# Optimization experiments

Measured on AMD Instinct MI355X. Metric: run time of the kernel, lower is better.

Reference implementation:

```python
import jax, jax.numpy as jnp
import numpy as np

NUM_BANDS = 31
POOL_SIZES = (4, 8, 16)
GN_GROUPS = 32
GN_EPS = 1e-5


def _interp_matrix(out_size, in_size):
    # PyTorch bilinear, align_corners=False, as a sparse-ish [out, in] matrix
    i = np.arange(out_size)
    src = (i + 0.5) * (in_size / out_size) - 0.5
    src = np.clip(src, 0.0, in_size - 1)
    lo = np.floor(src).astype(np.int64)
    hi = np.minimum(lo + 1, in_size - 1)
    w = src - lo
    M = np.zeros((out_size, in_size), dtype=np.float32)
    np.add.at(M, (i, lo), 1.0 - w)
    np.add.at(M, (i, hi), w)
    return jnp.asarray(M)


def _scale_branch(x, s, conv_w, spectral_w):
    # x: [B, C, H, W]; adaptive avg pool to (s, s) == uniform pooling (H, W % s == 0)
    B, C, H, W = x.shape
    xp = x.reshape(B, C, s, H // s, s, W // s).mean(axis=(3, 5))  # [B, C, s, s]
    qkv = jnp.einsum('bchw,oc->bohw', xp, conv_w)  # 1x1 conv, no bias
    rd = conv_w.shape[0] // 3
    q, k, v = qkv[:, :rd], qkv[:, rd:2 * rd], qkv[:, 2 * rd:]
    g = rd // NUM_BANDS  # bands_per_group
    S = s * s
    q = q.reshape(B, g, NUM_BANDS, S).transpose(0, 3, 1, 2)  # [B, S, g, n]
    k = k.reshape(B, g, NUM_BANDS, S).transpose(0, 3, 2, 1)  # [B, S, n, g]
    v = v.reshape(B, g, NUM_BANDS, S).transpose(0, 3, 1, 2)  # [B, S, g, n]
    scale = g ** (-0.5)
    attn = jnp.einsum('bsgn,nm,bsmh->bsgh', q, spectral_w, k) * scale  # [B, S, g, g]
    attn = jax.nn.softmax(attn, axis=-1)
    out = jnp.einsum('bsgh,bshn->bsgn', attn, v)  # [B, S, g, n]
    out = out.transpose(0, 2, 3, 1).reshape(B, rd, s, s)
    Mh = _interp_matrix(H, s)
    Mw = _interp_matrix(W, s)
    return jnp.einsum('bcij,hi,wj->bchw', out, Mh, Mw)  # bilinear upsample to [B, rd, H, W]


def _group_norm(x, weight, bias):
    B, C, H, W = x.shape
    xg = x.reshape(B, GN_GROUPS, C // GN_GROUPS, H, W)
    mean = xg.mean(axis=(2, 3, 4), keepdims=True)
    var = ((xg - mean) ** 2).mean(axis=(2, 3, 4), keepdims=True)
    xn = ((xg - mean) * jax.lax.rsqrt(var + GN_EPS)).reshape(B, C, H, W)
    return xn * weight[None, :, None, None] + bias[None, :, None, None]


def setup_inputs() -> dict:
    key = jax.random.key(0)
    ks = jax.random.split(key, 12)
    B, C, H, W = 4, 256, 256, 256
    rd = 93  # reduced_dim for dim=256, reduction=4, num_bands=31
    x = jax.random.normal(ks[0], (B, C, H, W), dtype=jnp.float32)
    conv_ws = [jax.random.normal(ks[1 + i], (3 * rd, C), dtype=jnp.float32) * (C ** -0.5) for i in range(3)]
    sws = [jnp.eye(NUM_BANDS, dtype=jnp.float32) * 0.1
           + 0.01 * jax.random.normal(ks[4 + i], (NUM_BANDS, NUM_BANDS), dtype=jnp.float32) for i in range(3)]
    fusion_w = jax.random.normal(ks[7], (C, 3 * rd), dtype=jnp.float32) * ((3 * rd) ** -0.5)
    fusion_b = jax.random.normal(ks[8], (C,), dtype=jnp.float32) * 0.01
    gn_w = jnp.ones((C,), dtype=jnp.float32) + 0.01 * jax.random.normal(ks[9], (C,), dtype=jnp.float32)
    gn_b = 0.01 * jax.random.normal(ks[10], (C,), dtype=jnp.float32)
    return {'x': x, 'conv_w0': conv_ws[0], 'conv_w1': conv_ws[1], 'conv_w2': conv_ws[2],
            'sw0': sws[0], 'sw1': sws[1], 'sw2': sws[2],
            'fusion_w': fusion_w, 'fusion_b': fusion_b, 'gn_w': gn_w, 'gn_b': gn_b}


def reference(x, conv_w0, conv_w1, conv_w2, sw0, sw1, sw2, fusion_w, fusion_b, gn_w, gn_b):
    conv_ws = (conv_w0, conv_w1, conv_w2)
    sws = (sw0, sw1, sw2)
    scale_outputs = [_scale_branch(x, s, cw, sw) for s, cw, sw in zip(POOL_SIZES, conv_ws, sws)]
    fused = jnp.concatenate(scale_outputs, axis=1)  # [B, 3*rd, H, W]
    out = jnp.einsum('bchw,oc->bohw', fused, fusion_w) + fusion_b[None, :, None, None]
    return _group_norm(out + x, gn_w, gn_b)
```

## Files before the change

### kernel.cpp

```cpp
#include <hip/hip_runtime.h>
#include <hip/hip_bf16.h>
#include <math.h>

#define B 4
#define C 256
#define H 256
#define Wd 256

__global__ __launch_bounds__(256) void xreadproj_kernel(
    const float* __restrict__ x,
    float* __restrict__ pool16, float* __restrict__ xp16o,
    float* __restrict__ xp8o, float* __restrict__ xp4o,
    float* __restrict__ sx) {

    __shared__ float P0[16][72];
    __shared__ float SS16[16][68];
    __shared__ float SS8[16][72];
    __shared__ float SS4[16][80];
    __shared__ float Rs[16 * 29];
    __shared__ float rs[4][2];

    int bc = blockIdx.x;
    int t = threadIdx.x;
    int wg = t >> 6, l = t & 63;

    const float4* xp = (const float4*)(x + (size_t)bc * (H * Wd));

    for (int e = t; e < 576; e += 256) {
        int r = e / 36, g = e - r * 36;
        if (g < 8)       P0[r][64 + g] = 0.f;
        else if (g < 10) SS16[r][g - 8] = 0.f;
        else if (g < 12) SS16[r][56 + g] = 0.f;
        else if (g < 16) SS8[r][g - 12] = 0.f;
        else if (g < 20) SS8[r][52 + g] = 0.f;
        else if (g < 28) SS4[r][g - 20] = 0.f;
        else             SS4[r][44 + g] = 0.f;
    }

    float a16, b16, a8, b8, a4, b4;
    {
        float w0 = 4.f * (float)l + 0.5f;
        float s16v = w0 * 0.0625f - 0.5f;
        if (l <= 1 || l >= 62) { a16 = 0.f; b16 = 0.f; }
        else { a16 = s16v - floorf(s16v); b16 = 0.0625f; }
        float s8v = w0 * 0.03125f - 0.5f;
        if (l <= 3 || l >= 60) { a8 = 0.f; b8 = 0.f; }
        else { a8 = s8v - floorf(s8v); b8 = 0.03125f; }
        float s4v = w0 * 0.015625f - 0.5f;
        if (l <= 7 || l >= 56) { a4 = 0.f; b4 = 0.f; }
        else { a4 = s4v - floorf(s4v); b4 = 0.015625f; }
    }

    const int i16 = t >> 4, j16 = t & 15;
    const int i8 = t >> 3, j8 = t & 7;
    const int i4 = (t - 64) >> 2, j4 = (t - 64) & 3;

    float accA = 0.f;
    float accB = 0.f;
    float sx1 = 0.f, sx2 = 0.f;

    float4 v[4], vn[4];
#pragma unroll
    for (int it = 0; it < 4; ++it)
        v[it] = xp[(wg * 4 + it) * 64 + l];

#pragma unroll 1
    for (int k = 0; k < 16; ++k) {
        if (k > 0) {
            int kk = k - 1;
            if (kk >= i16 - 1 && kk <= i16 + 1) {
#pragma unroll
                for (int rl = 0; rl < 16; ++rl) {
                    float src = ((float)(kk * 16 + rl) + 0.5f) * 0.0625f - 0.5f;
                    src = fminf(fmaxf(src, 0.f), 15.f);
                    int lo = (int)src; float fr = src - (float)lo;
                    float w = (i16 == lo) ? (1.f - fr) : ((i16 == lo + 1) ? fr : 0.f);
                    accA += w * Rs[rl * 29 + j16];
                }
            }
            if (t < 64) {
                if (kk >= 2 * i8 - 1 && kk <= 2 * i8 + 2) {
#pragma unroll
                    for (int rl = 0; rl < 16; ++rl) {
                        float src = ((float)(kk * 16 + rl) + 0.5f) * 0.03125f - 0.5f;
                        src = fminf(fmaxf(src, 0.f), 7.f);
                        int lo = (int)src; float fr = src - (float)lo;
                        float w = (i8 == lo) ? (1.f - fr) : ((i8 == lo + 1) ? fr : 0.f);
                        accB += w * Rs[rl * 29 + 16 + j8];
                    }
                }
            } else if (t < 80) {
                if (kk >= 4 * i4 - 2 && kk <= 4 * i4 + 5) {
#pragma unroll
                    for (int rl = 0; rl < 16; ++rl) {
                        float src = ((float)(kk * 16 + rl) + 0.5f) * 0.015625f - 0.5f;
                        src = fminf(fmaxf(src, 0.f), 3.f);
                        int lo = (int)src; float fr = src - (float)lo;
                        float w = (i4 == lo) ? (1.f - fr) : ((i4 == lo + 1) ? fr : 0.f);
                        accB += w * Rs[rl * 29 + 24 + j4];
                    }
                }
            }
        }

#pragma unroll
        for (int it = 0; it < 4; ++it) {
            int r = wg * 4 + it;
            float4 vv = v[it];
            float p0 = (vv.x + vv.y) + (vv.z + vv.w);
            float pw = fmaf(3.f, vv.w, fmaf(2.f, vv.z, vv.y));
            sx1 += p0;
            sx2 += vv.x * vv.x + vv.y * vv.y + vv.z * vv.z + vv.w * vv.w;
            P0[r][l]       = p0;
            SS16[r][2 + l] = fmaf(b16, pw, a16 * p0);
            SS8[r][4 + l]  = fmaf(b8,  pw, a8  * p0);
            SS4[r][8 + l]  = fmaf(b4,  pw, a4  * p0);
        }

        if (k < 15) {
#pragma unroll
            for (int it = 0; it < 4; ++it)
                vn[it] = xp[((k + 1) * 16 + wg * 4 + it) * 64 + l];
        }
        __syncthreads();

        for (int tk = t; tk < 464; tk += 256) {
            if (tk < 256) {
                int r = tk >> 4, j = tk & 15;
                float sum = 0.f;
#pragma unroll
                for (int q = 0; q < 4; ++q)
                    sum += P0[r][4 * j + 2 + q] - SS16[r][4 * j + 4 + q];
#pragma unroll
                for (int q = 0; q < 4; ++q) sum += SS16[r][4 * j + q];
                if (j == 0) sum += (P0[r][0] - SS16[r][2]) + (P0[r][1] - SS16[r][3]);
                Rs[r * 29 + j] = sum;
            } else if (tk < 384) {
                int q2 = tk - 256; int r = q2 >> 3, j = q2 & 7;
                float sum = 0.f;
#pragma unroll
                for (int q = 0; q < 8; ++q)
                    sum += P0[r][8 * j + 4 + q] - SS8[r][8 * j + 8 + q];
#pragma unroll
                for (int q = 0; q < 8; ++q) sum += SS8[r][8 * j + q];
                if (j == 0) {
#pragma unroll
                    for (int q = 0; q < 4; ++q) sum += P0[r][q] - SS8[r][4 + q];
                }
                Rs[r * 29 + 16 + j] = sum;
            } else if (tk < 448) {
                int q2 = tk - 384; int r = q2 >> 2, j = q2 & 3;
                float sum = 0.f;
#pragma unroll
                for (int q = 0; q < 16; ++q)
                    sum += P0[r][16 * j + 8 + q] - SS4[r][16 * j + 16 + q];
#pragma unroll
                for (int q = 0; q < 16; ++q) sum += SS4[r][16 * j + q];
                if (j == 0) {
#pragma unroll
                    for (int q = 0; q < 8; ++q) sum += P0[r][q] - SS4[r][8 + q];
                }
                Rs[r * 29 + 24 + j] = sum;
            } else {
                int j = tk - 448;
                float sum = 0.f;
#pragma unroll
                for (int r2 = 0; r2 < 16; ++r2) {
#pragma unroll
                    for (int q = 0; q < 4; ++q) sum += P0[r2][4 * j + q];
                }
                pool16[(size_t)bc * 256 + k * 16 + j] = sum * (1.f / 256.f);
            }
        }
        __syncthreads();
#pragma unroll
        for (int it = 0; it < 4; ++it) v[it] = vn[it];
    }

    {
        int kk = 15;
        if (kk >= i16 - 1 && kk <= i16 + 1) {
#pragma unroll
            for (int rl = 0; rl < 16; ++rl) {
                float src = ((float)(kk * 16 + rl) + 0.5f) * 0.0625f - 0.5f;
                src = fminf(fmaxf(src, 0.f), 15.f);
                int lo = (int)src; float fr = src - (float)lo;
                float w = (i16 == lo) ? (1.f - fr) : ((i16 == lo + 1) ? fr : 0.f);
                accA += w * Rs[rl * 29 + j16];
            }
        }
        if (t < 64) {
            if (kk >= 2 * i8 - 1 && kk <= 2 * i8 + 2) {
#pragma unroll
                for (int rl = 0; rl < 16; ++rl) {
                    float src = ((float)(kk * 16 + rl) + 0.5f) * 0.03125f - 0.5f;
                    src = fminf(fmaxf(src, 0.f), 7.f);
                    int lo = (int)src; float fr = src - (float)lo;
                    float w = (i8 == lo) ? (1.f - fr) : ((i8 == lo + 1) ? fr : 0.f);
                    accB += w * Rs[rl * 29 + 16 + j8];
                }
            }
        } else if (t < 80) {
            if (kk >= 4 * i4 - 2 && kk <= 4 * i4 + 5) {
#pragma unroll
                for (int rl = 0; rl < 16; ++rl) {
                    float src = ((float)(kk * 16 + rl) + 0.5f) * 0.015625f - 0.5f;
                    src = fminf(fmaxf(src, 0.f), 3.f);
                    int lo = (int)src; float fr = src - (float)lo;
                    float w = (i4 == lo) ? (1.f - fr) : ((i4 == lo + 1) ? fr : 0.f);
                    accB += w * Rs[rl * 29 + 24 + j4];
                }
            }
        }
    }

    xp16o[(size_t)bc * 256 + t] = accA;
    if (t < 64) xp8o[(size_t)bc * 64 + t] = accB;
    else if (t < 80) xp4o[(size_t)bc * 16 + (t - 64)] = accB;

#pragma unroll
    for (int off = 1; off < 64; off <<= 1) {
        sx1 += __shfl_xor(sx1, off);
        sx2 += __shfl_xor(sx2, off);
    }
    if (l == 0) { rs[wg][0] = sx1; rs[wg][1] = sx2; }
    __syncthreads();
    if (t == 0) {
        sx[bc * 2]     = rs[0][0] + rs[1][0] + rs[2][0] + rs[3][0];
        sx[bc * 2 + 1] = rs[0][1] + rs[1][1] + rs[2][1] + rs[3][1];
    }
}

__global__ __launch_bounds__(256) void site_kernel(
    const float* __restrict__ pool16,
    const float* __restrict__ cw0, const float* __restrict__ cw1,
    const float* __restrict__ cw2,
    const float* __restrict__ sw0, const float* __restrict__ sw1,
    const float* __restrict__ sw2,
    const float* __restrict__ fusion_w,
    float* __restrict__ y4, float* __restrict__ y8, float* __restrict__ y16) {

    __shared__ float P[256];
    __shared__ float Wm[961];
    __shared__ float QKV[279];
    __shared__ float QW[93];
    __shared__ float A[9];
    __shared__ float OUTV[93];

    int t = threadIdx.x;
    int blk = blockIdx.x;
    int b = blk / 336;
    int r = blk % 336;

    int s, site, foff;
    const float* cw; const float* sw; float* yout;
    if (r < 256)      { s = 16; site = r;       cw = cw2; sw = sw2; foff = 186; yout = y16; }
    else if (r < 320) { s = 8;  site = r - 256; cw = cw1; sw = sw1; foff = 93;  yout = y8;  }
    else              { s = 4;  site = r - 320; cw = cw0; sw = sw0; foff = 0;   yout = y4;  }
    int i = site / s, j = site % s;

    for (int idx = t; idx < 961; idx += 256) Wm[idx] = sw[idx];

    {
        int f = 16 / s;
        float acc = 0.f;
        int base = (b * 256 + t) * 256;
        for (int ii = 0; ii < f; ++ii)
            for (int jj = 0; jj < f; ++jj)
                acc += pool16[base + (i * f + ii) * 16 + (j * f + jj)];
        P[t] = acc / (float)(f * f);
    }
    __syncthreads();

    for (int o = t; o < 279; o += 256) {
        const float4* wrow = (const float4*)(cw + o * 256);
        float acc = 0.f;
#pragma unroll 8
        for (int c4 = 0; c4 < 64; ++c4) {
            float4 wv = wrow[c4];
            acc += wv.x * P[c4 * 4] + wv.y * P[c4 * 4 + 1] +
                   wv.z * P[c4 * 4 + 2] + wv.w * P[c4 * 4 + 3];
        }
        QKV[o] = acc;
    }
    __syncthreads();

    if (t < 93) {
        int g = t / 31, m = t % 31;
        float acc = 0.f;
        for (int n = 0; n < 31; ++n) acc += QKV[g * 31 + n] * Wm[n * 31 + m];
        QW[t] = acc;
    }
    __syncthreads();
    if (t < 9) {
        int g = t / 3, h = t % 3;
        float acc = 0.f;
        for (int m = 0; m < 31; ++m) acc += QW[g * 31 + m] * QKV[93 + h * 31 + m];
        A[t] = acc * 0.57735026918962576f;
    }
    __syncthreads();
    if (t < 3) {
        float a0 = A[t * 3], a1 = A[t * 3 + 1], a2 = A[t * 3 + 2];
        float mx = fmaxf(a0, fmaxf(a1, a2));
        float e0 = expf(a0 - mx), e1 = expf(a1 - mx), e2 = expf(a2 - mx);
        float inv = 1.0f / (e0 + e1 + e2);
        A[t * 3] = e0 * inv; A[t * 3 + 1] = e1 * inv; A[t * 3 + 2] = e2 * inv;
    }
    __syncthreads();
    if (t < 93) {
        int g = t / 31, n = t % 31;
        OUTV[t] = A[g * 3] * QKV[186 + n] + A[g * 3 + 1] * QKV[186 + 31 + n] +
                  A[g * 3 + 2] * QKV[186 + 62 + n];
    }
    __syncthreads();
    {
        const float* fr = fusion_w + t * 279 + foff;
        float acc = 0.f;
#pragma unroll 31
        for (int c = 0; c < 93; ++c) acc += fr[c] * OUTV[c];
        yout[(size_t)(b * 256 + t) * (s * s) + site] = acc;
    }
}

__global__ __launch_bounds__(256) void chanstat_kernel(
    const float* __restrict__ y4, const float* __restrict__ y8,
    const float* __restrict__ y16,
    const float* __restrict__ xp4, const float* __restrict__ xp8,
    const float* __restrict__ xp16,
    const float* __restrict__ sx, const float* __restrict__ fusion_b,
    double* __restrict__ chanS) {

    __shared__ float G1616[256], G168[128], G164[64], G88[64], G84[32], G44[16];
    __shared__ float cs[28];
    __shared__ float ybuf[336], xbuf[336];
    __shared__ float Tm[256];
    __shared__ float red[8];

    int t = threadIdx.x;
    int bc = blockIdx.x;

    for (int e = t; e < 588; e += 256) {
        if (e >= 560) {
            int q = e - 560; int sC, iC;
            if (q < 16) { sC = 16; iC = q; }
            else if (q < 24) { sC = 8; iC = q - 16; }
            else { sC = 4; iC = q - 24; }
            int R = 256 / sC;
            int lo = max(0, R * iC - R / 2), hi = min(256, R * iC + (3 * R) / 2);
            float Rinv = 1.f / (float)R, smax = (float)(sC - 1);
            float a = 0.f;
            for (int h = lo; h < hi; ++h) {
                float src = fminf(fmaxf(((float)h + 0.5f) * Rinv - 0.5f, 0.f), smax);
                int lq = (int)src; float fr = src - (float)lq;
                a += (iC == lq) ? (1.f - fr) : ((iC == lq + 1) ? fr : 0.f);
            }
            cs[q] = a;
            continue;
        }
        int sA, sB, iA, iB; float* dst; int off;
        if (e < 256)      { sA = 16; sB = 16; iA = e >> 4; iB = e & 15; dst = G1616; off = e; }
        else if (e < 384) { int q = e - 256; sA = 16; sB = 8; iA = q >> 3; iB = q & 7; dst = G168; off = q; }
        else if (e < 448) { int q = e - 384; sA = 16; sB = 4; iA = q >> 2; iB = q & 3; dst = G164; off = q; }
        else if (e < 512) { int q = e - 448; sA = 8;  sB = 8; iA = q >> 3; iB = q & 7; dst = G88;  off = q; }
        else if (e < 544) { int q = e - 512; sA = 8;  sB = 4; iA = q >> 2; iB = q & 3; dst = G84;  off = q; }
        else              { int q = e - 544; sA = 4;  sB = 4; iA = q >> 2; iB = q & 3; dst = G44;  off = q; }
        int RA = 256 / sA, RB = 256 / sB;
        int lo = max(max(0, RA * iA - RA / 2), RB * iB - RB / 2);
        int hi = min(min(256, RA * iA + (3 * RA) / 2), RB * iB + (3 * RB) / 2);
        float RAi = 1.f / (float)RA, RBi = 1.f / (float)RB;
        float smA = (float)(sA - 1), smB = (float)(sB - 1);
        float a = 0.f;
        for (int h = lo; h < hi; ++h) {
            float sa = fminf(fmaxf(((float)h + 0.5f) * RAi - 0.5f, 0.f), smA);
            int la = (int)sa; float fa = sa - (float)la;
            float wa = (iA == la) ? (1.f - fa) : ((iA == la + 1) ? fa : 0.f);
            float sb = fminf(fmaxf(((float)h + 0.5f) * RBi - 0.5f, 0.f), smB);
            int lb = (int)sb; float fb_ = sb - (float)lb;
            float wb = (iB == lb) ? (1.f - fb_) : ((iB == lb + 1) ? fb_ : 0.f);
            a += wa * wb;
        }
        dst[off] = a;
    }

    size_t bcs = (size_t)bc;
    ybuf[t] = y16[bcs * 256 + t];
    xbuf[t] = xp16[bcs * 256 + t];
    if (t < 64) { ybuf[256 + t] = y8[bcs * 64 + t]; xbuf[256 + t] = xp8[bcs * 64 + t]; }
    else if (t < 80) { ybuf[256 + t] = y4[bcs * 16 + (t - 64)]; xbuf[256 + t] = xp4[bcs * 16 + (t - 64)]; }
    __syncthreads();

    float pu = 0.f, pv = 0.f;
    for (int e = t; e < 336; e += 256) {
        float yv = ybuf[e];
        pv += 2.f * yv * xbuf[e];
        int ci, cj;
        if (e < 256)      { ci = e >> 4;               cj = e & 15; }
        else if (e < 320) { ci = 16 + ((e - 256) >> 3); cj = 16 + ((e - 256) & 7); }
        else              { ci = 24 + ((e - 320) >> 2); cj = 24 + ((e - 320) & 3); }
        pu += yv * cs[ci] * cs[cj];
    }

    for (int p = 0; p < 6; ++p) {
        const float* Gp; int sA, sB, yAoff, yBoff; float factor;
        switch (p) {
            case 0: Gp = G1616; sA = 16; sB = 16; yAoff = 0;   yBoff = 0;   factor = 1.f; break;
            case 1: Gp = G168;  sA = 16; sB = 8;  yAoff = 0;   yBoff = 256; factor = 2.f; break;
            case 2: Gp = G164;  sA = 16; sB = 4;  yAoff = 0;   yBoff = 320; factor = 2.f; break;
            case 3: Gp = G88;   sA = 8;  sB = 8;  yAoff = 256; yBoff = 256; factor = 1.f; break;
            case 4: Gp = G84;   sA = 8;  sB = 4;  yAoff = 256; yBoff = 320; factor = 2.f; break;
            default:Gp = G44;   sA = 4;  sB = 4;  yAoff = 320; yBoff = 320; factor = 1.f; break;
        }
        __syncthreads();
        int nT = sB * sA;
        if (t < nT) {
            int iB = t / sA, jA = t - iB * sA;
            float a = 0.f;
            for (int jB = 0; jB < sB; ++jB)
                a += Gp[jA * sB + jB] * ybuf[yBoff + iB * sB + jB];
            Tm[t] = a;
        }
        __syncthreads();
        int nB = sA * sA;
        if (t < nB) {
            int iA = t / sA, jA = t - iA * sA;
            float a = 0.f;
            for (int iB = 0; iB < sB; ++iB)
                a += Gp[iA * sB + iB] * Tm[iB * sA + jA];
            pv += factor * ybuf[yAoff + t] * a;
        }
    }

#pragma unroll
    for (int off = 1; off < 64; off <<= 1) {
        pu += __shfl_xor(pu, off);
        pv += __shfl_xor(pv, off);
    }
    __syncthreads();
    if ((t & 63) == 0) { red[(t >> 6) * 2] = pu; red[(t >> 6) * 2 + 1] = pv; }
    __syncthreads();
    if (t == 0) {
        float puT = red[0] + red[2] + red[4] + red[6];
        float pvT = red[1] + red[3] + red[5] + red[7];
        float fb = fusion_b[bc & 255];
        float s1 = sx[bc * 2], s2 = sx[bc * 2 + 1];
        double S1 = (double)s1 + 65536.0 * (double)fb + (double)puT;
        double S2 = (double)s2 + 2.0 * (double)fb * (double)s1 +
                    65536.0 * (double)fb * (double)fb +
                    2.0 * (double)fb * (double)puT + (double)pvT;
        chanS[bc * 2] = S1;
        chanS[bc * 2 + 1] = S2;
    }
}

__global__ __launch_bounds__(128) void gnfold_kernel(
    const double* __restrict__ chanS, float* __restrict__ stats_g) {
    int t = threadIdx.x;
    int b = t >> 5, g = t & 31;
    double gS1 = 0.0, gS2 = 0.0;
    for (int c8 = 0; c8 < 8; ++c8) {
        int c = g * 8 + c8;
        gS1 += chanS[(b * 256 + c) * 2];
        gS2 += chanS[(b * 256 + c) * 2 + 1];
    }
    double mean = gS1 / 524288.0;
    double var  = gS2 / 524288.0 - mean * mean;
    stats_g[t * 2] = (float)mean;
    stats_g[t * 2 + 1] = (float)(1.0 / sqrt(var + 1e-5));
}

__global__ __launch_bounds__(256) void write_kernel(
    const float* __restrict__ x,
    const float* __restrict__ ws_y4, const float* __restrict__ ws_y8,
    const float* __restrict__ ws_y16,
    const float* __restrict__ fusion_b,
    const float* __restrict__ gn_w, const float* __restrict__ gn_b,
    const float* __restrict__ stats_g,
    float* __restrict__ out) {

    __shared__ float ly16[256], ly8[64], ly4[16];
    __shared__ float2 rbd16[16][16];
    __shared__ float2 rbd8[16][8];
    __shared__ float2 rbd4[16][4];

    int blk = blockIdx.x;
    int hblk = blk & 15;
    int c = (blk >> 4) & 255;
    int b = blk >> 12;
    int t = threadIdx.x;

    ly16[t] = ws_y16[(size_t)(b * 256 + c) * 256 + t];
    if (t < 64) ly8[t] = ws_y8[(size_t)(b * 256 + c) * 64 + t];
    if (t < 16) ly4[t] = ws_y4[(size_t)(b * 256 + c) * 16 + t];
    __syncthreads();

    for (int idx = t; idx < 448; idx += 256) {
        int r = idx / 28;
        int q = idx - r * 28;
        int h = hblk * 16 + r;
        if (q < 16) {
            float src = (h + 0.5f) * 0.0625f - 0.5f;
            src = fminf(fmaxf(src, 0.f), 15.f);
            int lo = (int)src; float wf = src - lo; int hi = min(lo + 1, 15);
            float rb = (1.f - wf) * ly16[lo * 16 + q] + wf * ly16[hi * 16 + q];
            rbd16[r][q].x = rb;
            if (q > 0) rbd16[r][q - 1].y = rb;
            if (q == 15) rbd16[r][15].y = rb;
        } else if (q < 24) {
            int jj = q - 16;
            float src = (h + 0.5f) * 0.03125f - 0.5f;
            src = fminf(fmaxf(src, 0.f), 7.f);
            int lo = (int)src; float wf = src - lo; int hi = min(lo + 1, 7);
            float rb = (1.f - wf) * ly8[lo * 8 + jj] + wf * ly8[hi * 8 + jj];
            rbd8[r][jj].x = rb;
            if (jj > 0) rbd8[r][jj - 1].y = rb;
            if (jj == 7) rbd8[r][7].y = rb;
        } else {
            int jj = q - 24;
            float src = (h + 0.5f) * 0.015625f - 0.5f;
            src = fminf(fmaxf(src, 0.f), 3.f);
            int lo = (int)src; float wf = src - lo; int hi = min(lo + 1, 3);
            float rb = (1.f - wf) * ly4[lo * 4 + jj] + wf * ly4[hi * 4 + jj];
            rbd4[r][jj].x = rb;
            if (jj > 0) rbd4[r][jj - 1].y = rb;
            if (jj == 3) rbd4[r][3].y = rb;
        }
    }
    __syncthreads();

    int w4 = t & 63;
    int wg = t >> 6;
    int w0 = w4 * 4;

    int jlo16[4], jlo8[4], jlo4[4];
    float ww16[4], ww8[4], ww4[4];
#pragma unroll
    for (int p = 0; p < 4; ++p) {
        int w = w0 + p;
        float s16 = fminf(fmaxf((w + 0.5f) * 0.0625f - 0.5f, 0.f), 15.f);
        jlo16[p] = (int)s16; ww16[p] = s16 - jlo16[p];
        float s8 = fminf(fmaxf((w + 0.5f) * 0.03125f - 0.5f, 0.f), 7.f);
        jlo8[p] = (int)s8; ww8[p] = s8 - jlo8[p];
        float s4 = fminf(fmaxf((w + 0.5f) * 0.015625f - 0.5f, 0.f), 3.f);
        jlo4[p] = (int)s4; ww4[p] = s4 - jlo4[p];
    }

    float fb_c = fusion_b[c];
    int gidx = c >> 3;
    float mean = stats_g[(b * 32 + gidx) * 2];
    float rstd = stats_g[(b * 32 + gidx) * 2 + 1];
    float gwc = gn_w[c], gbc = gn_b[c];

    const float4* xp = (const float4*)(x + (size_t)(b * 256 + c) * (H * Wd));
    float4* op = (float4*)(out + (size_t)(b * 256 + c) * (H * Wd));

#pragma unroll
    for (int it = 0; it < 4; ++it) {
        int r = it * 4 + wg;
        int idx4 = (hblk * 16 + r) * 64 + w4;
        float4 xv = xp[idx4];
        float res[4];
        float px[4] = {xv.x, xv.y, xv.z, xv.w};
#pragma unroll
        for (int p = 0; p < 4; ++p) {
            float f = fb_c;
            float2 v16 = rbd16[r][jlo16[p]];
            f += (1.f - ww16[p]) * v16.x + ww16[p] * v16.y;
            float2 v8 = rbd8[r][jlo8[p]];
            f += (1.f - ww8[p]) * v8.x + ww8[p] * v8.y;
            float2 v4 = rbd4[r][jlo4[p]];
            f += (1.f - ww4[p]) * v4.x + ww4[p] * v4.y;
            float tv = px[p] + f;
            res[p] = (tv - mean) * rstd * gwc + gbc;
        }
        op[idx4] = make_float4(res[0], res[1], res[2], res[3]);
    }
}

extern "C" void kernel_launch(void* const* d_in, const int* in_sizes, int n_in,
                              void* d_out, int out_size, void* d_ws, size_t ws_size,
                              hipStream_t stream) {
    const float* x   = (const float*)d_in[0];
    const float* cw0 = (const float*)d_in[1];
    const float* cw1 = (const float*)d_in[2];
    const float* cw2 = (const float*)d_in[3];
    const float* sw0 = (const float*)d_in[4];
    const float* sw1 = (const float*)d_in[5];
    const float* sw2 = (const float*)d_in[6];
    const float* fw  = (const float*)d_in[7];
    const float* fb  = (const float*)d_in[8];
    const float* gw  = (const float*)d_in[9];
    const float* gb  = (const float*)d_in[10];
    float* out = (float*)d_out;

    float* ws     = (float*)d_ws;
    float* pool16 = ws;
    float* y4     = pool16 + 262144;
    float* y8     = y4 + 16384;
    float* y16    = y8 + 65536;
    float* xp16   = y16 + 262144;
    float* xp8    = xp16 + 262144;
    float* xp4    = xp8 + 65536;
    float* sx     = xp4 + 16384;
    float* statsg = sx + 2048;
    double* chanS = (double*)(statsg + 256);

    xreadproj_kernel<<<B * C, 256, 0, stream>>>(x, pool16, xp16, xp8, xp4, sx);
    site_kernel<<<B * 336, 256, 0, stream>>>(pool16, cw0, cw1, cw2,
                                             sw0, sw1, sw2, fw, y4, y8, y16);
    chanstat_kernel<<<B * C, 256, 0, stream>>>(y4, y8, y16, xp4, xp8, xp16,
                                               sx, fb, chanS);
    gnfold_kernel<<<1, 128, 0, stream>>>(chanS, statsg);
    write_kernel<<<B * C * 16, 256, 0, stream>>>(x, y4, y8, y16, fb, gw, gb,
                                                 statsg, out);
}
```

Baseline: 256.5 us.

## Split x-read projection kernel into four row-quarter blocks per channel

Each (batch, channel) plane is now handled by four blocks instead of one. Each block processes a quarter of the row strips and writes partial projections and sums to separate buffers, which chanstat then adds together. This gives the first pass four times more blocks and shorter serial loops, so the full 1024-block-per-launch memory read can spread over more CUs. The cost is larger partial workspace, a few extra reads in chanstat, and a possible issue at quarter boundaries: the k>0 check stops each block from adding its neighbour-strip contribution, so correctness depends on whether that partial term is complete.

```diff
diff --git a/kernel.cpp b/kernel.cpp
--- a/kernel.cpp
+++ b/kernel.cpp
@@ -9,9 +9,9 @@
 
 __global__ __launch_bounds__(256) void xreadproj_kernel(
     const float* __restrict__ x,
-    float* __restrict__ pool16, float* __restrict__ xp16o,
-    float* __restrict__ xp8o, float* __restrict__ xp4o,
-    float* __restrict__ sx) {
+    float* __restrict__ pool16,
+    float* __restrict__ xpp16, float* __restrict__ xpp8,
+    float* __restrict__ xpp4, float* __restrict__ sxp) {
 
     __shared__ float P0[16][72];
     __shared__ float SS16[16][68];
@@ -20,7 +20,9 @@
     __shared__ float Rs[16 * 29];
     __shared__ float rs[4][2];
 
-    int bc = blockIdx.x;
+    int blk = blockIdx.x;
+    int qb = blk & 3;
+    int bc = blk >> 2;
     int t = threadIdx.x;
     int wg = t >> 6, l = t & 63;
 
@@ -62,12 +64,14 @@
     float4 v[4], vn[4];
 #pragma unroll
     for (int it = 0; it < 4; ++it)
-        v[it] = xp[(wg * 4 + it) * 64 + l];
+        v[it] = xp[((qb * 4) * 16 + wg * 4 + it) * 64 + l];
 
 #pragma unroll 1
-    for (int k = 0; k < 16; ++k) {
+    for (int k = 0; k < 4; ++k) {
+        int kg = qb * 4 + k;
+
         if (k > 0) {
-            int kk = k - 1;
+            int kk = kg - 1;
             if (kk >= i16 - 1 && kk <= i16 + 1) {
 #pragma unroll
                 for (int rl = 0; rl < 16; ++rl) {
@@ -117,10 +121,10 @@
             SS4[r][8 + l]  = fmaf(b4,  pw, a4  * p0);
         }
 
-        if (k < 15) {
+        if (k < 3) {
 #pragma unroll
             for (int it = 0; it < 4; ++it)
-                vn[it] = xp[((k + 1) * 16 + wg * 4 + it) * 64 + l];
+                vn[it] = xp[((kg + 1) * 16 + wg * 4 + it) * 64 + l];
         }
         __syncthreads();
 
@@ -169,7 +173,7 @@
 #pragma unroll
                     for (int q = 0; q < 4; ++q) sum += P0[r2][4 * j + q];
                 }
-                pool16[(size_t)bc * 256 + k * 16 + j] = sum * (1.f / 256.f);
+                pool16[(size_t)bc * 256 + kg * 16 + j] = sum * (1.f / 256.f);
             }
         }
         __syncthreads();
@@ -178,7 +182,7 @@
     }
 
     {
-        int kk = 15;
+        int kk = qb * 4 + 3;
         if (kk >= i16 - 1 && kk <= i16 + 1) {
 #pragma unroll
             for (int rl = 0; rl < 16; ++rl) {
@@ -214,9 +218,10 @@
         }
     }
 
-    xp16o[(size_t)bc * 256 + t] = accA;
-    if (t < 64) xp8o[(size_t)bc * 64 + t] = accB;
-    else if (t < 80) xp4o[(size_t)bc * 16 + (t - 64)] = accB;
+    size_t pbase = (size_t)qb * 1024 + bc;
+    xpp16[pbase * 256 + t] = accA;
+    if (t < 64) xpp8[pbase * 64 + t] = accB;
+    else if (t < 80) xpp4[pbase * 16 + (t - 64)] = accB;
 
 #pragma unroll
     for (int off = 1; off < 64; off <<= 1) {
@@ -226,8 +231,8 @@
     if (l == 0) { rs[wg][0] = sx1; rs[wg][1] = sx2; }
     __syncthreads();
     if (t == 0) {
-        sx[bc * 2]     = rs[0][0] + rs[1][0] + rs[2][0] + rs[3][0];
-        sx[bc * 2 + 1] = rs[0][1] + rs[1][1] + rs[2][1] + rs[3][1];
+        sxp[pbase * 2]     = rs[0][0] + rs[1][0] + rs[2][0] + rs[3][0];
+        sxp[pbase * 2 + 1] = rs[0][1] + rs[1][1] + rs[2][1] + rs[3][1];
     }
 }
 
@@ -325,9 +330,9 @@
 __global__ __launch_bounds__(256) void chanstat_kernel(
     const float* __restrict__ y4, const float* __restrict__ y8,
     const float* __restrict__ y16,
-    const float* __restrict__ xp4, const float* __restrict__ xp8,
-    const float* __restrict__ xp16,
-    const float* __restrict__ sx, const float* __restrict__ fusion_b,
+    const float* __restrict__ xpp4, const float* __restrict__ xpp8,
+    const float* __restrict__ xpp16,
+    const float* __restrict__ sxp, const float* __restrict__ fusion_b,
     double* __restrict__ chanS) {
 
     __shared__ float G1616[256], G168[128], G164[64], G88[64], G84[32], G44[16];
@@ -384,9 +389,28 @@
 
     size_t bcs = (size_t)bc;
     ybuf[t] = y16[bcs * 256 + t];
-    xbuf[t] = xp16[bcs * 256 + t];
-    if (t < 64) { ybuf[256 + t] = y8[bcs * 64 + t]; xbuf[256 + t] = xp8[bcs * 64 + t]; }
-    else if (t < 80) { ybuf[256 + t] = y4[bcs * 16 + (t - 64)]; xbuf[256 + t] = xp4[bcs * 16 + (t - 64)]; }
+    {
+        float xb = 0.f;
+#pragma unroll
+        for (int q = 0; q < 4; ++q)
+            xb += xpp16[((size_t)q * 1024 + bcs) * 256 + t];
+        xbuf[t] = xb;
+    }
+    if (t < 64) {
+        ybuf[256 + t] = y8[bcs * 64 + t];
+        float xb = 0.f;
+#pragma unroll
+        for (int q = 0; q < 4; ++q)
+            xb += xpp8[((size_t)q * 1024 + bcs) * 64 + t];
+        xbuf[256 + t] = xb;
+    } else if (t < 80) {
+        ybuf[256 + t] = y4[bcs * 16 + (t - 64)];
+        float xb = 0.f;
+#pragma unroll
+        for (int q = 0; q < 4; ++q)
+            xb += xpp4[((size_t)q * 1024 + bcs) * 16 + (t - 64)];
+        xbuf[256 + t] = xb;
+    }
     __syncthreads();
 
     float pu = 0.f, pv = 0.f;
@@ -442,7 +466,12 @@
         float puT = red[0] + red[2] + red[4] + red[6];
         float pvT = red[1] + red[3] + red[5] + red[7];
         float fb = fusion_b[bc & 255];
-        float s1 = sx[bc * 2], s2 = sx[bc * 2 + 1];
+        float s1 = 0.f, s2 = 0.f;
+#pragma unroll
+        for (int q = 0; q < 4; ++q) {
+            s1 += sxp[((size_t)q * 1024 + bcs) * 2];
+            s2 += sxp[((size_t)q * 1024 + bcs) * 2 + 1];
+        }
         double S1 = (double)s1 + 65536.0 * (double)fb + (double)puT;
         double S2 = (double)s2 + 2.0 * (double)fb * (double)s1 +
                     65536.0 * (double)fb * (double)fb +
@@ -597,18 +626,19 @@
     float* y4     = pool16 + 262144;
     float* y8     = y4 + 16384;
     float* y16    = y8 + 65536;
-    float* xp16   = y16 + 262144;
-    float* xp8    = xp16 + 262144;
-    float* xp4    = xp8 + 65536;
-    float* sx     = xp4 + 16384;
-    float* statsg = sx + 2048;
+    float* xpp16  = y16 + 262144;
+    float* xpp8   = xpp16 + 1048576;
+    float* xpp4   = xpp8 + 262144;
+    float* sxp    = xpp4 + 65536;
+    float* statsg = sxp + 8192;
     double* chanS = (double*)(statsg + 256);
 
-    xreadproj_kernel<<<B * C, 256, 0, stream>>>(x, pool16, xp16, xp8, xp4, sx);
+    xreadproj_kernel<<<B * C * 4, 256, 0, stream>>>(x, pool16, xpp16, xpp8,
+                                                    xpp4, sxp);
     site_kernel<<<B * 336, 256, 0, stream>>>(pool16, cw0, cw1, cw2,
                                              sw0, sw1, sw2, fw, y4, y8, y16);
-    chanstat_kernel<<<B * C, 256, 0, stream>>>(y4, y8, y16, xp4, xp8, xp16,
-                                               sx, fb, chanS);
+    chanstat_kernel<<<B * C, 256, 0, stream>>>(y4, y8, y16, xpp4, xpp8, xpp16,
+                                               sxp, fb, chanS);
     gnfold_kernel<<<1, 128, 0, stream>>>(chanS, statsg);
     write_kernel<<<B * C * 16, 256, 0, stream>>>(x, y4, y8, y16, fb, gw, gb,
                                                  statsg, out);
```

Measured after the change: 267.9 us. 1.04x slower.
